# Kernel tuning notes

Hardware: AMD Instinct MI355X
Metric: run time of the kernel (lower is better)

The kernel has to match this reference:

```python
import jax, jax.numpy as jnp
import numpy as np

B = 131072
INP, HID, NEXP, OUT = 5, 64, 40, 5


def setup_inputs() -> dict:
    key = jax.random.key(0)
    ks = jax.random.split(key, 9)
    s = lambda fan_in: 1.0 / np.sqrt(fan_in)
    return {
        "x": jax.random.normal(ks[0], (B, INP), dtype=jnp.float32),
        "enc_w": jax.random.uniform(ks[1], (INP, HID), jnp.float32, -s(INP), s(INP)),
        "enc_b": jax.random.uniform(ks[2], (HID,), jnp.float32, -s(INP), s(INP)),
        "triz_w": jax.random.uniform(ks[3], (NEXP, HID, HID), jnp.float32, -s(HID), s(HID)),
        "triz_b": jax.random.uniform(ks[4], (NEXP, HID), jnp.float32, -s(HID), s(HID)),
        "pol_w": jax.random.uniform(ks[5], (HID, NEXP), jnp.float32, -s(HID), s(HID)),
        "pol_b": jax.random.uniform(ks[6], (NEXP,), jnp.float32, -s(HID), s(HID)),
        "dec_w": jax.random.uniform(ks[7], (HID, OUT), jnp.float32, -s(HID), s(HID)),
        "dec_b": jax.random.uniform(ks[8], (OUT,), jnp.float32, -s(HID), s(HID)),
    }


def reference(x, enc_w, enc_b, triz_w, triz_b, pol_w, pol_b, dec_w, dec_b):
    # Encoder: tanh(Linear)
    z = jnp.tanh(x @ enc_w + enc_b)                       # [B, 64]
    # TRIZLayer: dense 40-expert Linear+ReLU, stacked on axis 1
    h = jax.nn.relu(jnp.einsum('bd,edf->bef', z, triz_w) + triz_b[None])  # [B, 40, 64]
    # Policy: softmax logits -> categorical sample
    logits = z @ pol_w + pol_b                            # [B, 40]
    probs = jax.nn.softmax(logits, axis=-1)
    actions = jax.random.categorical(jax.random.key(1), logits, axis=-1)  # [B]
    # Gather the sampled expert's output per token
    selected = jnp.take_along_axis(h, actions[:, None, None], axis=1)[:, 0]  # [B, 64]
    out = selected @ dec_w + dec_b                        # [B, 5]
    return (out, probs, actions, h)
```

## Files before the change

kernel.cpp:

```cpp
#include <hip/hip_runtime.h>
#include <stdint.h>
#include <math.h>

#define B_ROWS 131072
#define INP 5
#define HID 64
#define NEXP 40
#define OUT_D 5

typedef short bf16x8 __attribute__((ext_vector_type(8)));
typedef float f32x16 __attribute__((ext_vector_type(16)));

__device__ __forceinline__ uint32_t rotl32(uint32_t v, int d) {
  return (v << d) | (v >> (32 - d));
}

__device__ __forceinline__ void threefry2x32(uint32_t ks0, uint32_t ks1,
                                             uint32_t x0, uint32_t x1,
                                             uint32_t& o0, uint32_t& o1) {
  uint32_t ks2 = ks0 ^ ks1 ^ 0x1BD11BDAu;
  x0 += ks0; x1 += ks1;
  x0 += x1; x1 = rotl32(x1, 13); x1 ^= x0;
  x0 += x1; x1 = rotl32(x1, 15); x1 ^= x0;
  x0 += x1; x1 = rotl32(x1, 26); x1 ^= x0;
  x0 += x1; x1 = rotl32(x1, 6);  x1 ^= x0;
  x0 += ks1; x1 += ks2 + 1u;
  x0 += x1; x1 = rotl32(x1, 17); x1 ^= x0;
  x0 += x1; x1 = rotl32(x1, 29); x1 ^= x0;
  x0 += x1; x1 = rotl32(x1, 16); x1 ^= x0;
  x0 += x1; x1 = rotl32(x1, 24); x1 ^= x0;
  x0 += ks2; x1 += ks0 + 2u;
  x0 += x1; x1 = rotl32(x1, 13); x1 ^= x0;
  x0 += x1; x1 = rotl32(x1, 15); x1 ^= x0;
  x0 += x1; x1 = rotl32(x1, 26); x1 ^= x0;
  x0 += x1; x1 = rotl32(x1, 6);  x1 ^= x0;
  x0 += ks0; x1 += ks1 + 3u;
  x0 += x1; x1 = rotl32(x1, 17); x1 ^= x0;
  x0 += x1; x1 = rotl32(x1, 29); x1 ^= x0;
  x0 += x1; x1 = rotl32(x1, 16); x1 ^= x0;
  x0 += x1; x1 = rotl32(x1, 24); x1 ^= x0;
  x0 += ks1; x1 += ks2 + 4u;
  x0 += x1; x1 = rotl32(x1, 13); x1 ^= x0;
  x0 += x1; x1 = rotl32(x1, 15); x1 ^= x0;
  x0 += x1; x1 = rotl32(x1, 26); x1 ^= x0;
  x0 += x1; x1 = rotl32(x1, 6);  x1 ^= x0;
  x0 += ks2; x1 += ks0 + 5u;
  o0 = x0; o1 = x1;
}

__device__ __forceinline__ uint16_t f32_to_bf16(float f) {
  uint32_t u = __float_as_uint(f);
  u += 0x7fffu + ((u >> 16) & 1u);
  return (uint16_t)(u >> 16);
}

__global__ __launch_bounds__(256) void pack_w_kernel(
    const float* __restrict__ triz_w, uint16_t* __restrict__ wp) {
  int i = blockIdx.x * 256 + threadIdx.x;
  if (i >= NEXP * HID * HID) return;
  int e = i >> 12;
  int rem = i & 4095;
  int k = rem >> 6;
  int f = rem & 63;
  int kk = k >> 4, kl = k & 15;
  int half = kl >> 3, j = kl & 7;
  int nt = f >> 5;
  int lane = half * 32 + (f & 31);
  int dst = ((((e * 4 + kk) * 2 + nt) * 64) + lane) * 8 + j;
  wp[dst] = f32_to_bf16(triz_w[i]);
}

__global__ __launch_bounds__(256) void enc_policy_kernel(
    const float* __restrict__ x, const float* __restrict__ enc_w,
    const float* __restrict__ enc_b, const float* __restrict__ pol_w,
    const float* __restrict__ pol_b, uint16_t* __restrict__ z_bf16,
    int* __restrict__ actions_i, float* __restrict__ probs_out,
    float* __restrict__ actions_f) {
  const int lane = threadIdx.x & 63;
  const int gw = blockIdx.x * 4 + (threadIdx.x >> 6);
  const int je = lane < NEXP ? lane : NEXP - 1;

  float ew[INP];
#pragma unroll
  for (int d = 0; d < INP; ++d) ew[d] = enc_w[d * HID + lane];
  const double eb = (double)enc_b[lane];
  float pw[HID];
#pragma unroll
  for (int j = 0; j < HID; ++j) pw[j] = pol_w[j * NEXP + je];
  const double pb = (double)pol_b[je];

  const int r0 = gw * 32;
  for (int r = r0; r < r0 + 32; ++r) {
    double a = eb;
#pragma unroll
    for (int d = 0; d < INP; ++d)
      a += (double)x[r * INP + d] * (double)ew[d];
    double z = tanh(a);
    z_bf16[(size_t)r * HID + lane] = f32_to_bf16((float)z);

    double l0 = 0.0, l1 = 0.0, l2 = 0.0, l3 = 0.0;
#pragma unroll
    for (int j = 0; j < HID; j += 4) {
      l0 += __shfl(z, j + 0) * (double)pw[j + 0];
      l1 += __shfl(z, j + 1) * (double)pw[j + 1];
      l2 += __shfl(z, j + 2) * (double)pw[j + 2];
      l3 += __shfl(z, j + 3) * (double)pw[j + 3];
    }
    double logit = pb + ((l0 + l1) + (l2 + l3));

    uint32_t idx = (uint32_t)r * NEXP + (uint32_t)je;
    uint32_t o0, o1;
    threefry2x32(0u, 1u, 0u, idx, o0, o1);
    uint32_t bits = o0 ^ o1;
    const float TINY = 1.17549435e-38f;
    float uf = __uint_as_float((bits >> 9) | 0x3f800000u) - 1.0f;
    uf = uf * (1.0f - TINY) + TINY;
    uf = fmaxf(uf, TINY);
    double g = -log(-log((double)uf));
    double val = logit + g;

    double mv = (lane < NEXP) ? val : -1.0e300;
    int mi = (lane < NEXP) ? lane : 64;
#pragma unroll
    for (int off = 32; off > 0; off >>= 1) {
      double ov = __shfl_down(mv, off);
      int oi = __shfl_down(mi, off);
      if (ov > mv || (ov == mv && oi < mi)) { mv = ov; mi = oi; }
    }
    mi = __shfl(mi, 0);
    if (lane == 0) {
      actions_i[r] = mi;
      actions_f[r] = (float)mi;
    }

    double lm = (lane < NEXP) ? logit : -1.0e300;
#pragma unroll
    for (int off = 32; off > 0; off >>= 1) {
      double ov = __shfl_down(lm, off);
      lm = ov > lm ? ov : lm;
    }
    lm = __shfl(lm, 0);
    double p = (lane < NEXP) ? exp(logit - lm) : 0.0;
    double s = p;
#pragma unroll
    for (int off = 32; off > 0; off >>= 1) s += __shfl_down(s, off);
    s = __shfl(s, 0);
    if (lane < NEXP) probs_out[(size_t)r * NEXP + lane] = (float)(p / s);
  }
}

__global__ __launch_bounds__(256) void triz_kernel(
    const uint16_t* __restrict__ z_bf16, const uint16_t* __restrict__ wp,
    const float* __restrict__ triz_b, float* __restrict__ h) {
  const int lane = threadIdx.x & 63;
  const int wv = threadIdx.x >> 6;
  const int m0 = blockIdx.x * 128 + wv * 32;
  const int half = lane >> 5;
  const int col = lane & 31;

  const uint16_t* zr = z_bf16 + (size_t)(m0 + col) * HID + half * 8;
  bf16x8 A[4];
#pragma unroll
  for (int kk = 0; kk < 4; ++kk)
    A[kk] = *reinterpret_cast<const bf16x8*>(zr + kk * 16);

  float* hb = h + (size_t)(m0 + (half << 2)) * (NEXP * HID) + col;

  const bf16x8* wpv = reinterpret_cast<const bf16x8*>(wp);
  for (int e = 0; e < NEXP; ++e) {
    const bf16x8* wpe = wpv + (size_t)e * 512 + lane;
    f32x16 acc0 = {}, acc1 = {};
#pragma unroll
    for (int kk = 0; kk < 4; ++kk) {
      bf16x8 b0 = wpe[(kk * 2 + 0) * 64];
      bf16x8 b1 = wpe[(kk * 2 + 1) * 64];
      acc0 = __builtin_amdgcn_mfma_f32_32x32x16_bf16(A[kk], b0, acc0, 0, 0, 0);
      acc1 = __builtin_amdgcn_mfma_f32_32x32x16_bf16(A[kk], b1, acc1, 0, 0, 0);
    }
    float bv0 = triz_b[e * HID + col];
    float bv1 = triz_b[e * HID + 32 + col];
#pragma unroll
    for (int reg = 0; reg < 16; ++reg) {
      int row = (reg & 3) + ((reg >> 2) << 3);
      size_t off = (size_t)row * (NEXP * HID) + (size_t)e * HID;
      hb[off] = fmaxf(acc0[reg] + bv0, 0.0f);
      hb[off + 32] = fmaxf(acc1[reg] + bv1, 0.0f);
    }
  }
}

__global__ __launch_bounds__(256) void decode_kernel(
    const float* __restrict__ h, const int* __restrict__ actions_i,
    const float* __restrict__ dec_w, const float* __restrict__ dec_b,
    float* __restrict__ out) {
  int b = blockIdx.x * 256 + threadIdx.x;
  if (b >= B_ROWS) return;
  int a = actions_i[b];
  const float4* hr =
      reinterpret_cast<const float4*>(h + ((size_t)b * NEXP + a) * HID);
  float acc0 = dec_b[0], acc1 = dec_b[1], acc2 = dec_b[2], acc3 = dec_b[3],
        acc4 = dec_b[4];
#pragma unroll
  for (int q = 0; q < 16; ++q) {
    float4 hv = hr[q];
#pragma unroll
    for (int t = 0; t < 4; ++t) {
      float v = (&hv.x)[t];
      int f = q * 4 + t;
      acc0 += v * dec_w[f * 5 + 0];
      acc1 += v * dec_w[f * 5 + 1];
      acc2 += v * dec_w[f * 5 + 2];
      acc3 += v * dec_w[f * 5 + 3];
      acc4 += v * dec_w[f * 5 + 4];
    }
  }
  float* o = out + (size_t)b * OUT_D;
  o[0] = acc0; o[1] = acc1; o[2] = acc2; o[3] = acc3; o[4] = acc4;
}

extern "C" void kernel_launch(void* const* d_in, const int* in_sizes, int n_in,
                              void* d_out, int out_size, void* d_ws,
                              size_t ws_size, hipStream_t stream) {
  const float* x = (const float*)d_in[0];
  const float* enc_w = (const float*)d_in[1];
  const float* enc_b = (const float*)d_in[2];
  const float* triz_w = (const float*)d_in[3];
  const float* triz_b = (const float*)d_in[4];
  const float* pol_w = (const float*)d_in[5];
  const float* pol_b = (const float*)d_in[6];
  const float* dec_w = (const float*)d_in[7];
  const float* dec_b = (const float*)d_in[8];

  float* out = (float*)d_out;
  float* probs = out + (size_t)B_ROWS * OUT_D;
  float* actions_f = probs + (size_t)B_ROWS * NEXP;
  float* h = actions_f + B_ROWS;

  uint8_t* ws = (uint8_t*)d_ws;
  uint16_t* z_bf16 = (uint16_t*)ws;
  uint16_t* wpack = (uint16_t*)(ws + (size_t)B_ROWS * HID * 2);
  int* actions_i =
      (int*)(ws + (size_t)B_ROWS * HID * 2 + (size_t)NEXP * HID * HID * 2);

  pack_w_kernel<<<(NEXP * HID * HID + 255) / 256, 256, 0, stream>>>(triz_w,
                                                                    wpack);
  enc_policy_kernel<<<B_ROWS / 128, 256, 0, stream>>>(
      x, enc_w, enc_b, pol_w, pol_b, z_bf16, actions_i, probs, actions_f);
  triz_kernel<<<B_ROWS / 128, 256, 0, stream>>>(z_bf16, wpack, triz_b, h);
  decode_kernel<<<B_ROWS / 256, 256, 0, stream>>>(h, actions_i, dec_w, dec_b,
                                                  out);
}
```

Baseline: 1.845 ms.

## Compute encoder and policy in fp32 per-row with fp64 fixup for near-tie samples

Rewrites the encoder/policy kernel so that each thread handles one row in fp32 with fast tanh, log and exp, replacing the per-wave fp64 shuffle reductions. It tracks the top-two Gumbel scores and records rows whose margin is below a threshold in a list. A new fixup kernel recomputes those rows in fp64 so the sampled action still matches the reference. It also transposes the weights once, reuses the h output buffer as scratch before triz overwrites it, and makes the h stores nontemporal. The risk is that fp32 errors larger than the margin, or list overflow, could change sampled actions.

```diff
diff --git a/kernel.cpp b/kernel.cpp
--- a/kernel.cpp
+++ b/kernel.cpp
@@ -7,6 +7,9 @@
 #define HID 64
 #define NEXP 40
 #define OUT_D 5
+
+#define MARGIN 4e-3f
+#define LISTCAP 16384
 
 typedef short bf16x8 __attribute__((ext_vector_type(8)));
 typedef float f32x16 __attribute__((ext_vector_type(16)));
@@ -54,10 +57,104 @@
   return (uint16_t)(u >> 16);
 }
 
+__device__ __forceinline__ float rcpf_fast(float d) {
+  float r = __builtin_amdgcn_rcpf(d);
+  r = fmaf(r, fmaf(-d, r, 1.0f), r);
+  return r;
+}
+
+__device__ __forceinline__ double rcp64_fast(double y) {
+  double r = __builtin_amdgcn_rcp(y);
+  r = fma(r, fma(-y, r, 1.0), r);
+  r = fma(r, fma(-y, r, 1.0), r);
+  return r;
+}
+
+__device__ __forceinline__ float tanhf_fast(float a) {
+  float t = __expf(2.0f * a);
+  float d = t + 1.0f;
+  return fmaf(-2.0f, rcpf_fast(d), 1.0f);
+}
+
+__device__ __forceinline__ double flog64s(double xx) {
+  long long b = __double_as_longlong(xx);
+  int e = (int)(b >> 52) - 1023;
+  double m = __longlong_as_double((b & 0xFFFFFFFFFFFFFLL) | 0x3FF0000000000000LL);
+  if (m > 1.4142135623730951) { m *= 0.5; e += 1; }
+  double t = (m - 1.0) * rcp64_fast(m + 1.0);
+  double t2 = t * t;
+  double p = fma(t2, fma(t2, 1.42857142857142857e-01, 2.0e-01),
+                 3.33333333333333333e-01);
+  double q = 2.0 * t;
+  double lm = fma(q * t2, p, q);
+  return fma((double)e, 6.93147180559945309e-01, lm);
+}
+
+__device__ __forceinline__ double flog64(double xx) {
+  long long b = __double_as_longlong(xx);
+  int e = (int)(b >> 52) - 1023;
+  double m = __longlong_as_double((b & 0xFFFFFFFFFFFFFLL) | 0x3FF0000000000000LL);
+  if (m > 1.4142135623730951) { m *= 0.5; e += 1; }
+  double t = (m - 1.0) * rcp64_fast(m + 1.0);
+  double t2 = t * t;
+  double p = 7.69230769230769231e-02;
+  p = fma(p, t2, 9.09090909090909091e-02);
+  p = fma(p, t2, 1.11111111111111111e-01);
+  p = fma(p, t2, 1.42857142857142857e-01);
+  p = fma(p, t2, 2.0e-01);
+  p = fma(p, t2, 3.33333333333333333e-01);
+  double q = 2.0 * t;
+  double lm = fma(q * t2, p, q);
+  double ed = (double)e;
+  return fma(ed, 6.93147180369123816490e-01,
+             fma(ed, 1.90821492927058770002e-10, lm));
+}
+
+__device__ __forceinline__ double fexp64(double xx) {
+  double t = xx * 1.44269504088896340736;
+  double n = rint(t);
+  double r = fma(-n, 6.93147180369123816490e-01, xx);
+  r = fma(-n, 1.90821492927058770002e-10, r);
+  double p = 2.08767569878680989792e-09;
+  p = fma(p, r, 2.50521083854417187751e-08);
+  p = fma(p, r, 2.75573192239858906526e-07);
+  p = fma(p, r, 2.75573192239858925110e-06);
+  p = fma(p, r, 2.48015873015873015873e-05);
+  p = fma(p, r, 1.98412698412698412698e-04);
+  p = fma(p, r, 1.38888888888888894068e-03);
+  p = fma(p, r, 8.33333333333333321769e-03);
+  p = fma(p, r, 4.16666666666666666435e-02);
+  p = fma(p, r, 1.66666666666666657415e-01);
+  p = fma(p, r, 5.0e-01);
+  p = fma(p, r, 1.0);
+  p = fma(p, r, 1.0);
+  int ni = (int)n;
+  double s = __longlong_as_double((long long)(1023 + ni) << 52);
+  return p * s;
+}
+
+__device__ __forceinline__ double tanh64_fast(double a) {
+  double t = fexp64(2.0 * a);
+  return fma(-2.0, rcp64_fast(t + 1.0), 1.0);
+}
+
 __global__ __launch_bounds__(256) void pack_w_kernel(
-    const float* __restrict__ triz_w, uint16_t* __restrict__ wp) {
+    const float* __restrict__ triz_w, uint16_t* __restrict__ wp,
+    const float* __restrict__ pol_w, const float* __restrict__ enc_w,
+    float* __restrict__ pwT, float* __restrict__ ewT, int* __restrict__ cnt) {
+  if (blockIdx.x == 640) {
+    for (int t = threadIdx.x; t < NEXP * HID; t += 256) {
+      int e = t >> 6, j = t & 63;
+      pwT[e * 64 + j] = pol_w[j * NEXP + e];
+    }
+    for (int t = threadIdx.x; t < 512; t += 256) {
+      int j = t >> 3, d = t & 7;
+      ewT[t] = (d < INP) ? enc_w[d * HID + j] : 0.0f;
+    }
+    if (threadIdx.x == 0) *cnt = 0;
+    return;
+  }
   int i = blockIdx.x * 256 + threadIdx.x;
-  if (i >= NEXP * HID * HID) return;
   int e = i >> 12;
   int rem = i & 4095;
   int k = rem >> 6;
@@ -71,81 +168,154 @@
 }
 
 __global__ __launch_bounds__(256) void enc_policy_kernel(
-    const float* __restrict__ x, const float* __restrict__ enc_w,
-    const float* __restrict__ enc_b, const float* __restrict__ pol_w,
+    const float* __restrict__ x, const float* __restrict__ ewT,
+    const float* __restrict__ enc_b, const float* __restrict__ pwT,
     const float* __restrict__ pol_b, uint16_t* __restrict__ z_bf16,
     int* __restrict__ actions_i, float* __restrict__ probs_out,
-    float* __restrict__ actions_f) {
-  const int lane = threadIdx.x & 63;
-  const int gw = blockIdx.x * 4 + (threadIdx.x >> 6);
-  const int je = lane < NEXP ? lane : NEXP - 1;
-
-  float ew[INP];
-#pragma unroll
-  for (int d = 0; d < INP; ++d) ew[d] = enc_w[d * HID + lane];
-  const double eb = (double)enc_b[lane];
-  float pw[HID];
-#pragma unroll
-  for (int j = 0; j < HID; ++j) pw[j] = pol_w[j * NEXP + je];
-  const double pb = (double)pol_b[je];
-
-  const int r0 = gw * 32;
-  for (int r = r0; r < r0 + 32; ++r) {
-    double a = eb;
-#pragma unroll
-    for (int d = 0; d < INP; ++d)
-      a += (double)x[r * INP + d] * (double)ew[d];
-    double z = tanh(a);
-    z_bf16[(size_t)r * HID + lane] = f32_to_bf16((float)z);
-
-    double l0 = 0.0, l1 = 0.0, l2 = 0.0, l3 = 0.0;
-#pragma unroll
-    for (int j = 0; j < HID; j += 4) {
-      l0 += __shfl(z, j + 0) * (double)pw[j + 0];
-      l1 += __shfl(z, j + 1) * (double)pw[j + 1];
-      l2 += __shfl(z, j + 2) * (double)pw[j + 2];
-      l3 += __shfl(z, j + 3) * (double)pw[j + 3];
-    }
-    double logit = pb + ((l0 + l1) + (l2 + l3));
-
-    uint32_t idx = (uint32_t)r * NEXP + (uint32_t)je;
+    float* __restrict__ actions_f, int* __restrict__ cnt,
+    int* __restrict__ list) {
+  __shared__ float lgs[256 * 41];
+  const int r = blockIdx.x * 256 + threadIdx.x;
+
+  const float xv0 = x[r * INP + 0], xv1 = x[r * INP + 1],
+              xv2 = x[r * INP + 2], xv3 = x[r * INP + 3],
+              xv4 = x[r * INP + 4];
+
+  float z[64];
+#pragma unroll
+  for (int j = 0; j < 64; ++j) {
+    const float4 w = *reinterpret_cast<const float4*>(ewT + j * 8);
+    const float w4 = ewT[j * 8 + 4];
+    float a = enc_b[j];
+    a = fmaf(xv0, w.x, a);
+    a = fmaf(xv1, w.y, a);
+    a = fmaf(xv2, w.z, a);
+    a = fmaf(xv3, w.w, a);
+    a = fmaf(xv4, w4, a);
+    z[j] = tanhf_fast(a);
+  }
+
+  {
+    uint32_t zb[32];
+#pragma unroll
+    for (int p = 0; p < 32; ++p)
+      zb[p] = (uint32_t)f32_to_bf16(z[2 * p]) |
+              ((uint32_t)f32_to_bf16(z[2 * p + 1]) << 16);
+    uint4* zo = reinterpret_cast<uint4*>(z_bf16 + (size_t)r * HID);
+#pragma unroll
+    for (int q = 0; q < 8; ++q)
+      zo[q] = make_uint4(zb[4 * q], zb[4 * q + 1], zb[4 * q + 2], zb[4 * q + 3]);
+  }
+
+  float* mylg = lgs + threadIdx.x * 41;
+  float best = -1e30f, second = -1e30f;
+  int bi = 0;
+#pragma unroll 2
+  for (int e = 0; e < NEXP; ++e) {
+    const float4* wp4 = reinterpret_cast<const float4*>(pwT + e * 64);
+    float a0 = 0.f, a1 = 0.f, a2 = 0.f, a3 = 0.f;
+#pragma unroll
+    for (int q = 0; q < 16; ++q) {
+      float4 w = wp4[q];
+      a0 = fmaf(z[4 * q + 0], w.x, a0);
+      a1 = fmaf(z[4 * q + 1], w.y, a1);
+      a2 = fmaf(z[4 * q + 2], w.z, a2);
+      a3 = fmaf(z[4 * q + 3], w.w, a3);
+    }
+    float lg = pol_b[e] + ((a0 + a1) + (a2 + a3));
+    mylg[e] = lg;
+
     uint32_t o0, o1;
-    threefry2x32(0u, 1u, 0u, idx, o0, o1);
+    threefry2x32(0u, 1u, 0u, (uint32_t)r * NEXP + (uint32_t)e, o0, o1);
     uint32_t bits = o0 ^ o1;
     const float TINY = 1.17549435e-38f;
     float uf = __uint_as_float((bits >> 9) | 0x3f800000u) - 1.0f;
     uf = uf * (1.0f - TINY) + TINY;
     uf = fmaxf(uf, TINY);
-    double g = -log(-log((double)uf));
-    double val = logit + g;
-
-    double mv = (lane < NEXP) ? val : -1.0e300;
-    int mi = (lane < NEXP) ? lane : 64;
-#pragma unroll
-    for (int off = 32; off > 0; off >>= 1) {
-      double ov = __shfl_down(mv, off);
-      int oi = __shfl_down(mi, off);
-      if (ov > mv || (ov == mv && oi < mi)) { mv = ov; mi = oi; }
-    }
-    mi = __shfl(mi, 0);
-    if (lane == 0) {
-      actions_i[r] = mi;
-      actions_f[r] = (float)mi;
-    }
-
-    double lm = (lane < NEXP) ? logit : -1.0e300;
-#pragma unroll
-    for (int off = 32; off > 0; off >>= 1) {
-      double ov = __shfl_down(lm, off);
-      lm = ov > lm ? ov : lm;
-    }
-    lm = __shfl(lm, 0);
-    double p = (lane < NEXP) ? exp(logit - lm) : 0.0;
-    double s = p;
-#pragma unroll
-    for (int off = 32; off > 0; off >>= 1) s += __shfl_down(s, off);
-    s = __shfl(s, 0);
-    if (lane < NEXP) probs_out[(size_t)r * NEXP + lane] = (float)(p / s);
+    double v = -flog64s((double)uf);
+    float g = -__logf((float)v);
+
+    float val = lg + g;
+    if (val > best) {
+      second = best; best = val; bi = e;
+    } else if (val > second) {
+      second = val;
+    }
+  }
+
+  actions_i[r] = bi;
+  actions_f[r] = (float)bi;
+  if (best - second < MARGIN) {
+    int slot = atomicAdd(cnt, 1);
+    if (slot < LISTCAP) list[slot] = r;
+  }
+
+  float mx = -1e30f;
+  for (int e = 0; e < NEXP; ++e) mx = fmaxf(mx, mylg[e]);
+  float s = 0.f;
+  for (int e = 0; e < NEXP; ++e) {
+    float p = __expf(mylg[e] - mx);
+    mylg[e] = p;
+    s += p;
+  }
+  float inv = rcpf_fast(s);
+  float4* po = reinterpret_cast<float4*>(probs_out + (size_t)r * NEXP);
+  for (int k = 0; k < 10; ++k) {
+    float4 pv;
+    pv.x = mylg[4 * k + 0] * inv;
+    pv.y = mylg[4 * k + 1] * inv;
+    pv.z = mylg[4 * k + 2] * inv;
+    pv.w = mylg[4 * k + 3] * inv;
+    po[k] = pv;
+  }
+}
+
+__global__ __launch_bounds__(256) void fixup_kernel(
+    const float* __restrict__ x, const float* __restrict__ ewT,
+    const float* __restrict__ enc_b, const float* __restrict__ pwT,
+    const float* __restrict__ pol_b, const int* __restrict__ cnt,
+    const int* __restrict__ list, int* __restrict__ actions_i,
+    float* __restrict__ actions_f) {
+  int n = *cnt;
+  if (n > LISTCAP) n = LISTCAP;
+  for (int ii = blockIdx.x * blockDim.x + threadIdx.x; ii < n;
+       ii += gridDim.x * blockDim.x) {
+    int r = list[ii];
+    double zd[64];
+#pragma unroll
+    for (int j = 0; j < 64; ++j) {
+      double a = (double)enc_b[j];
+#pragma unroll
+      for (int d = 0; d < INP; ++d)
+        a += (double)x[r * INP + d] * (double)ewT[j * 8 + d];
+      zd[j] = tanh64_fast(a);
+    }
+    double best = -1.0e300;
+    int bi = 0;
+    for (int e = 0; e < NEXP; ++e) {
+      double a0 = 0.0, a1 = 0.0, a2 = 0.0, a3 = 0.0;
+#pragma unroll
+      for (int j = 0; j < 64; j += 4) {
+        a0 += zd[j + 0] * (double)pwT[e * 64 + j + 0];
+        a1 += zd[j + 1] * (double)pwT[e * 64 + j + 1];
+        a2 += zd[j + 2] * (double)pwT[e * 64 + j + 2];
+        a3 += zd[j + 3] * (double)pwT[e * 64 + j + 3];
+      }
+      double lg = (double)pol_b[e] + ((a0 + a1) + (a2 + a3));
+      uint32_t o0, o1;
+      threefry2x32(0u, 1u, 0u, (uint32_t)r * NEXP + (uint32_t)e, o0, o1);
+      uint32_t bits = o0 ^ o1;
+      const float TINY = 1.17549435e-38f;
+      float uf = __uint_as_float((bits >> 9) | 0x3f800000u) - 1.0f;
+      uf = uf * (1.0f - TINY) + TINY;
+      uf = fmaxf(uf, TINY);
+      double v = -flog64((double)uf);
+      double g = -flog64(v);
+      double val = lg + g;
+      if (val > best) { best = val; bi = e; }
+    }
+    actions_i[r] = bi;
+    actions_f[r] = (float)bi;
   }
 }
 
@@ -183,8 +353,8 @@
     for (int reg = 0; reg < 16; ++reg) {
       int row = (reg & 3) + ((reg >> 2) << 3);
       size_t off = (size_t)row * (NEXP * HID) + (size_t)e * HID;
-      hb[off] = fmaxf(acc0[reg] + bv0, 0.0f);
-      hb[off + 32] = fmaxf(acc1[reg] + bv1, 0.0f);
+      __builtin_nontemporal_store(fmaxf(acc0[reg] + bv0, 0.0f), &hb[off]);
+      __builtin_nontemporal_store(fmaxf(acc1[reg] + bv1, 0.0f), &hb[off + 32]);
     }
   }
 }
@@ -242,10 +412,18 @@
   int* actions_i =
       (int*)(ws + (size_t)B_ROWS * HID * 2 + (size_t)NEXP * HID * HID * 2);
 
-  pack_w_kernel<<<(NEXP * HID * HID + 255) / 256, 256, 0, stream>>>(triz_w,
-                                                                    wpack);
-  enc_policy_kernel<<<B_ROWS / 128, 256, 0, stream>>>(
-      x, enc_w, enc_b, pol_w, pol_b, z_bf16, actions_i, probs, actions_f);
+  float* pwT = h;
+  float* ewT = pwT + NEXP * HID;
+  int* cnt = (int*)(ewT + 512);
+  int* list = cnt + 1;
+
+  pack_w_kernel<<<641, 256, 0, stream>>>(triz_w, wpack, pol_w, enc_w, pwT,
+                                         ewT, cnt);
+  enc_policy_kernel<<<B_ROWS / 256, 256, 0, stream>>>(
+      x, ewT, enc_b, pwT, pol_b, z_bf16, actions_i, probs, actions_f, cnt,
+      list);
+  fixup_kernel<<<32, 256, 0, stream>>>(x, ewT, enc_b, pwT, pol_b, cnt, list,
+                                       actions_i, actions_f);
   triz_kernel<<<B_ROWS / 128, 256, 0, stream>>>(z_bf16, wpack, triz_b, h);
   decode_kernel<<<B_ROWS / 256, 256, 0, stream>>>(h, actions_i, dec_w, dec_b,
                                                   out);
```

Measured after the change: 1.588 ms. -13.9%, faster.
